# Kernel tuning notes

Hardware: AMD Instinct MI355X
Metric: run time of the kernel (lower is better)

Reference implementation:

```python
import jax, jax.numpy as jnp
import numpy as np

D_MODEL = 64
LN_EPS = 1e-5


def _conv1d(x, w, b, stride, pad):
    # x: (B, Cin, L), w: (Cout, Cin, K)
    y = jax.lax.conv_general_dilated(x, w, (stride,), [(pad, pad)],
                                     dimension_numbers=('NCH', 'OIH', 'NCH'))
    return y + b[None, :, None]


def _layernorm(x, g, b):
    # normalize over last dim (feature dim), matching nn.LayerNorm(d_model)
    m = jnp.mean(x, axis=-1, keepdims=True)
    v = jnp.var(x, axis=-1, keepdims=True)
    return (x - m) * jax.lax.rsqrt(v + LN_EPS) * g + b


def _pos_embed(L, d):
    pos = jnp.arange(L, dtype=jnp.float32)[:, None]
    div = jnp.exp(jnp.arange(0, d, 2, dtype=jnp.float32) * (-np.log(10000.0) / d))
    pe = jnp.zeros((L, d), jnp.float32)
    pe = pe.at[:, 0::2].set(jnp.sin(pos * div))
    pe = pe.at[:, 1::2].set(jnp.cos(pos * div))
    return pe


def setup_inputs():
    key = jax.random.key(0)
    ks = jax.random.split(key, 20)
    B, L, D = 128, 4096, D_MODEL
    G = D // 4  # 16 convs per kernel-size group (kernels cycle [3,5,7,9])
    inp = {'x': jax.random.normal(ks[0], (B, 1, L), jnp.float32)}
    kernels = [3, 5, 7, 9]
    for i, k in enumerate(kernels):
        fan = float(1.0 / np.sqrt(k))
        inp['tok_w%d' % k] = jax.random.uniform(ks[1 + 2 * i], (G, 1, k), jnp.float32, -fan, fan)
        inp['tok_b%d' % k] = jax.random.uniform(ks[2 + 2 * i], (G,), jnp.float32, -fan, fan)
    fan = float(1.0 / np.sqrt(D * 4))
    for j in range(3):
        inp['c_w%d' % (j + 1)] = jax.random.uniform(ks[10 + 2 * j], (D, D, 4), jnp.float32, -fan, fan)
        inp['c_b%d' % (j + 1)] = jax.random.uniform(ks[11 + 2 * j], (D,), jnp.float32, -fan, fan)
    for j in range(2):
        inp['ln_g%d' % (j + 1)] = jnp.ones((D,), jnp.float32)
        inp['ln_b%d' % (j + 1)] = jnp.zeros((D,), jnp.float32)
    return inp


def reference(x, tok_w3, tok_b3, tok_w5, tok_b5, tok_w7, tok_b7, tok_w9, tok_b9,
              c_w1, c_b1, c_w2, c_b2, c_w3, c_b3, ln_g1, ln_b1, ln_g2, ln_b2):
    B, _, L = x.shape
    D = D_MODEL
    # TokenEmbedding: conv i has kernel [3,5,7,9][i%4]; fuse the d_model 1-channel
    # convs into 4 grouped convs (one per kernel size), then interleave channels.
    outs = [
        _conv1d(x, tok_w3, tok_b3, 1, 1),
        _conv1d(x, tok_w5, tok_b5, 1, 2),
        _conv1d(x, tok_w7, tok_b7, 1, 3),
        _conv1d(x, tok_w9, tok_b9, 1, 4),
    ]  # each (B, D//4, L); group g holds channels i with i % 4 == g, ordered by i // 4
    emb = jnp.stack(outs, axis=2).reshape(B, D, L)  # channel i = (i//4)*4 + (i%4)
    # add sinusoidal positional embedding (dropout is identity in eval mode)
    h = emb + _pos_embed(L, D).T[None]  # (B, D, L)
    # CompressionEmbedding: conv(k=4, s=2, p=1) -> tanh -> LN (over D) chain
    h = jnp.tanh(_conv1d(h, c_w1, c_b1, 2, 1))
    h = _layernorm(h.transpose(0, 2, 1), ln_g1, ln_b1).transpose(0, 2, 1)
    h = jnp.tanh(_conv1d(h, c_w2, c_b2, 2, 1))
    h = _layernorm(h.transpose(0, 2, 1), ln_g2, ln_b2).transpose(0, 2, 1)
    h = jnp.tanh(_conv1d(h, c_w3, c_b3, 2, 1))
    return h.transpose(0, 2, 1)  # (B, L//8, D)
```

## Files before the change

kernel.cpp:

```cpp
#include <hip/hip_runtime.h>
#include <math.h>

#define BATCH 128
#define LN_EPS 1e-5f

typedef short bf16x8 __attribute__((ext_vector_type(8)));
typedef short bf16x4 __attribute__((ext_vector_type(4)));
typedef float f32x4  __attribute__((ext_vector_type(4)));

__device__ __forceinline__ ushort f2bf(float f) {
    return __builtin_bit_cast(ushort, (__bf16)f);
}

__device__ __forceinline__ float fast_tanh(float v) {
    float e = __expf(2.f * v);
    return 1.f - 2.f / (e + 1.f);
}

__global__ __launch_bounds__(256, 2)
void prep_kernel(const float* __restrict__ cw1, const float* __restrict__ cw2,
                 const float* __restrict__ cw3,
                 const float* __restrict__ w3, const float* __restrict__ b3,
                 const float* __restrict__ w5, const float* __restrict__ b5,
                 const float* __restrict__ w7, const float* __restrict__ b7,
                 const float* __restrict__ w9, const float* __restrict__ b9,
                 const float* __restrict__ cb1, const float* __restrict__ cb2,
                 const float* __restrict__ cb3,
                 const float* __restrict__ lg1, const float* __restrict__ lb1,
                 const float* __restrict__ lg2, const float* __restrict__ lb2,
                 ushort* __restrict__ Wm23, ushort* __restrict__ Wm1,
                 float* __restrict__ W0c, float* __restrict__ W3c,
                 float* __restrict__ pe1c,
                 float* __restrict__ cb2t, float* __restrict__ B2k0,
                 float* __restrict__ B2k3,
                 float* __restrict__ cb3t, float* __restrict__ B3k0,
                 float* __restrict__ B3k3) {
    const int tid = threadIdx.x;
    const int bx  = blockIdx.x;
    const int idx = bx * 256 + tid;

    __shared__ float tile[64][132];
    __shared__ float red[4][64][24];
    __shared__ float cbred[64][4];

    {
        int s = idx >> 14, r = idx & 16383;
        int j = r & 7, l15 = (r >> 3) & 15, dt = (r >> 7) & 3;
        int quad = (r >> 9) & 3, k2 = (r >> 11) & 1, kk = (r >> 12) & 3;
        int dout = dt * 16 + l15, din = k2 * 32 + quad * 8 + j;
        const float* cw = (s == 0) ? cw2 : cw3;
        const float* lg = (s == 0) ? lg1 : lg2;
        Wm23[idx] = f2bf(cw[dout * 256 + din * 4 + kk] * lg[din]);
    }

    if (bx == 1 && tid < 128) {
        const int s = tid >> 6, ch = tid & 63;
        const float* cw = (s == 0) ? cw2 : cw3;
        const float* lb = (s == 0) ? lb1 : lb2;
        float full = 0.f, k0 = 0.f, k3 = 0.f;
        for (int din = 0; din < 64; ++din) {
            float bv = lb[din];
            const float* wr = cw + ch * 256 + din * 4;
            k0 = fmaf(wr[0], bv, k0);
            k3 = fmaf(wr[3], bv, k3);
            full = fmaf(wr[0] + wr[1] + wr[2] + wr[3], bv, full);
        }
        if (s == 0) { cb2t[ch] = cb2[ch] + full; B2k0[ch] = k0; B2k3[ch] = k3; }
        else        { cb3t[ch] = cb3[ch] + full; B3k0[ch] = k0; B3k3[ch] = k3; }
    }

    if (bx == 0) {
        const int ch = tid & 63, part = tid >> 6;
        const float* cw1row = cw1 + ch * 256;
        float acc[24];
#pragma unroll
        for (int j = 0; j < 24; ++j) acc[j] = 0.f;
        for (int din = part * 16; din < part * 16 + 16; ++din) {
            int ki = din & 3, g = din >> 2;
            float wl[9];
#pragma unroll
            for (int j = 0; j < 9; ++j) wl[j] = 0.f;
            float bias;
            if (ki == 0)      { for (int j = 0; j < 3; ++j) wl[3 + j] = w3[g * 3 + j]; bias = b3[g]; }
            else if (ki == 1) { for (int j = 0; j < 5; ++j) wl[2 + j] = w5[g * 5 + j]; bias = b5[g]; }
            else if (ki == 2) { for (int j = 0; j < 7; ++j) wl[1 + j] = w7[g * 7 + j]; bias = b7[g]; }
            else              { for (int j = 0; j < 9; ++j) wl[j]     = w9[g * 9 + j]; bias = b9[g]; }
#pragma unroll
            for (int kk = 0; kk < 4; ++kk) {
                float c = cw1row[din * 4 + kk];
                acc[12 + kk] += c * bias;
#pragma unroll
                for (int u = 0; u < 9; ++u) acc[kk + u] += c * wl[u];
            }
            float c0 = cw1row[din * 4 + 0], c3 = cw1row[din * 4 + 3];
#pragma unroll
            for (int u = 0; u < 4; ++u) { acc[16 + u] += c0 * wl[5 + u]; acc[20 + u] += c3 * wl[u]; }
        }
#pragma unroll
        for (int j = 0; j < 24; ++j) red[part][ch][j] = acc[j];
    }

    {
        const int pair = tid & 63, part = tid >> 6;
        const int kk = pair >> 4, chl = pair & 15;
        const int ch = (bx & 3) * 16 + chl;
        float s = 0.f;
        for (int din = part * 16; din < part * 16 + 16; ++din) {
            int ki = din & 3, g = din >> 2;
            float bias = (ki == 0) ? b3[g] : (ki == 1) ? b5[g] : (ki == 2) ? b7[g] : b9[g];
            s += cw1[ch * 256 + din * 4 + kk] * bias;
        }
        cbred[pair][part] = s;
    }

    const int l0 = (bx >> 2) * 64;
    const int pin0 = 2 * l0 - 1;
    for (int i2 = tid; i2 < 64 * 130; i2 += 256) {
        int d = i2 / 130, pp = i2 - d * 130;
        int p = pin0 + pp;
        float v = 0.f;
        if (p >= 0 && p < 4096) {
            float dv = __expf((float)(d & ~1) * -0.14391156831212787f);
            float ang = (float)p * dv;
            v = (d & 1) ? __cosf(ang) : __sinf(ang);
        }
        tile[d][pp] = v;
    }
    __syncthreads();

    if (bx == 0 && tid < 64) {
        const int ch = tid;
        float w24[24];
#pragma unroll
        for (int j = 0; j < 24; ++j)
            w24[j] = red[0][ch][j] + red[1][ch][j] + red[2][ch][j] + red[3][ch][j];
        int dt = ch >> 4, l15 = ch & 15;
#pragma unroll
        for (int quad = 0; quad < 4; ++quad)
#pragma unroll
            for (int j = 0; j < 8; ++j) {
                int k = quad * 8 + j;
                Wm1[((quad * 4 + dt) * 16 + l15) * 8 + j] = f2bf(k < 12 ? w24[k] : 0.f);
            }
#pragma unroll
        for (int u = 0; u < 4; ++u) { W0c[ch * 4 + u] = w24[16 + u]; W3c[ch * 4 + u] = w24[20 + u]; }
    }

    const int lane = tid & 63, wv = tid >> 6;
    const int l = l0 + lane;
    const int chl0 = wv * 4;
    const int db = (bx & 3) * 16 + chl0;
    float a4[4];
#pragma unroll
    for (int j = 0; j < 4; ++j) {
        int chl = chl0 + j;
        float cbk0 = cbred[0 * 16 + chl][0] + cbred[0 * 16 + chl][1] + cbred[0 * 16 + chl][2] + cbred[0 * 16 + chl][3];
        float cbk1 = cbred[1 * 16 + chl][0] + cbred[1 * 16 + chl][1] + cbred[1 * 16 + chl][2] + cbred[1 * 16 + chl][3];
        float cbk2 = cbred[2 * 16 + chl][0] + cbred[2 * 16 + chl][1] + cbred[2 * 16 + chl][2] + cbred[2 * 16 + chl][3];
        float cbk3 = cbred[3 * 16 + chl][0] + cbred[3 * 16 + chl][1] + cbred[3 * 16 + chl][2] + cbred[3 * 16 + chl][3];
        float a = cb1[db + j] + cbk1 + cbk2;
        if (l > 0) a += cbk0;
        if (l < 2047) a += cbk3;
        a4[j] = a;
    }
    for (int din = 0; din < 64; ++din) {
        float v0 = tile[din][2 * lane + 0], v1 = tile[din][2 * lane + 1];
        float v2 = tile[din][2 * lane + 2], v3 = tile[din][2 * lane + 3];
        const float* wb = cw1 + din * 4;
#pragma unroll
        for (int j = 0; j < 4; ++j) {
            const float* wj = wb + (db + j) * 256;
            a4[j] = fmaf(v0, wj[0], fmaf(v1, wj[1], fmaf(v2, wj[2], fmaf(v3, wj[3], a4[j]))));
        }
    }
    *(float4*)(pe1c + (size_t)l * 64 + db) = make_float4(a4[0], a4[1], a4[2], a4[3]);
}

__global__ __launch_bounds__(256, 2)
void mega_kernel(const float* __restrict__ x,
                 const ushort* __restrict__ Wm1, const ushort* __restrict__ Wm23,
                 const float* __restrict__ pe1c,
                 const float* __restrict__ W0c, const float* __restrict__ W3c,
                 const float* __restrict__ cb2t, const float* __restrict__ B2k0,
                 const float* __restrict__ B2k3,
                 const float* __restrict__ cb3t, const float* __restrict__ B3k0,
                 const float* __restrict__ B3k3,
                 float* __restrict__ out) {
    const int b = blockIdx.y;
    const int g0 = blockIdx.x * 64;
    const int tid = threadIdx.x;

    __shared__ __align__(16) ushort xs[640];
    __shared__ __align__(16) ushort TE1[148][72];
    __shared__ __align__(16) ushort TO1[148][72];
    __shared__ __align__(16) ushort TE2[66][72];
    __shared__ __align__(16) ushort TO2[66][72];

    for (int i = tid; i < 640; i += 256) {
        int g = 8 * g0 - 11 + i;
        float v = (g >= 0 && g < 4096) ? x[b * 4096 + g] : 0.f;
        xs[i] = f2bf(v);
    }
    __syncthreads();

    const int wv = tid >> 6, lane = tid & 63;
    const int quad = lane >> 4, l15 = lane & 15;

    {
        bf16x8 afr1[4];
#pragma unroll
        for (int dt = 0; dt < 4; ++dt)
            afr1[dt] = *(const bf16x8*)&Wm1[((quad * 4 + dt) * 16 + l15) * 8];
        const int qstart = 4 * g0 - 3;
        for (int pass = wv; pass < 9; pass += 4) {
            const int mb = pass * 32;
            f32x4 a1[2][4];
#pragma unroll
            for (int pt = 0; pt < 2; ++pt) {
                const int m = mb + pt * 16 + l15;
                const int q = qstart + m;
                const int qc = (q < 0) ? 0 : ((q > 2047) ? 2047 : q);
                const float* pb_ = pe1c + (size_t)qc * 64 + quad * 4;
#pragma unroll
                for (int dt = 0; dt < 4; ++dt) {
                    float4 pv = *(const float4*)(pb_ + dt * 16);
                    a1[pt][dt][0] = pv.x; a1[pt][dt][1] = pv.y;
                    a1[pt][dt][2] = pv.z; a1[pt][dt][3] = pv.w;
                }
                union { bf16x8 v; unsigned u[4]; } tmp;
                const unsigned* p = (const unsigned*)&xs[2 * m + 8 * quad];
#pragma unroll
                for (int i = 0; i < 4; ++i) tmp.u[i] = p[i];
#pragma unroll
                for (int dt = 0; dt < 4; ++dt)
                    a1[pt][dt] = __builtin_amdgcn_mfma_f32_16x16x32_bf16(
                        afr1[dt], tmp.v, a1[pt][dt], 0, 0, 0);
            }
#pragma unroll
            for (int pt = 0; pt < 2; ++pt) {
                const int m = mb + pt * 16 + l15;
                if (m >= 264) continue;
                const int q = qstart + m;
                ushort* dst = (m & 1) ? &TE1[(m + 1) >> 1][0] : &TO1[m >> 1][0];
                if (q >= 0 && q < 2048) {
                    if (q == 0 || q == 2047) {
                        const float* Wc = (q == 0) ? W0c : W3c;
                        const float* xe = x + b * 4096 + ((q == 0) ? 0 : 4092);
                        float x0 = xe[0], x1 = xe[1], x2 = xe[2], x3 = xe[3];
#pragma unroll
                        for (int dt = 0; dt < 4; ++dt)
#pragma unroll
                            for (int r = 0; r < 4; ++r) {
                                const float* wc = Wc + (dt * 16 + quad * 4 + r) * 4;
                                a1[pt][dt][r] -= wc[0] * x0 + wc[1] * x1 + wc[2] * x2 + wc[3] * x3;
                            }
                    }
                    float s = 0.f, s2 = 0.f;
#pragma unroll
                    for (int dt = 0; dt < 4; ++dt)
#pragma unroll
                        for (int r = 0; r < 4; ++r) {
                            float t = fast_tanh(a1[pt][dt][r]);
                            s += t;
                            s2 = fmaf(t, t, s2);
                        }
                    s += __shfl_xor(s, 16, 64);
                    s += __shfl_xor(s, 32, 64);
                    s2 += __shfl_xor(s2, 16, 64);
                    s2 += __shfl_xor(s2, 32, 64);
                    float mean = s * 0.015625f;
                    float var = fmaf(-mean, mean, s2 * 0.015625f);
                    float rstd = rsqrtf(var + LN_EPS);
                    float nmr = -mean * rstd;
#pragma unroll
                    for (int dt = 0; dt < 4; ++dt) {
                        bf16x4 pk;
#pragma unroll
                        for (int r = 0; r < 4; ++r)
                            pk[r] = (short)f2bf(fmaf(fast_tanh(a1[pt][dt][r]), rstd, nmr));
                        *(bf16x4*)(dst + dt * 16 + quad * 4) = pk;
                    }
                } else {
                    bf16x4 z; z[0] = 0; z[1] = 0; z[2] = 0; z[3] = 0;
#pragma unroll
                    for (int dt = 0; dt < 4; ++dt)
                        *(bf16x4*)(dst + dt * 16 + quad * 4) = z;
                }
            }
        }
    }
    __syncthreads();

    for (int pass = wv; pass < 9; pass += 4) {
        const int n = pass * 16 + l15;
        f32x4 a2[4];
#pragma unroll
        for (int dt = 0; dt < 4; ++dt) {
            float4 cv = *(const float4*)(cb2t + dt * 16 + quad * 4);
            a2[dt][0] = cv.x; a2[dt][1] = cv.y; a2[dt][2] = cv.z; a2[dt][3] = cv.w;
        }
#pragma unroll
        for (int kk = 0; kk < 4; ++kk) {
            const ushort (*T)[72] = (kk & 1) ? TE1 : TO1;
            const int row = n + ((kk + 1) >> 1);
#pragma unroll
            for (int k2 = 0; k2 < 2; ++k2) {
                bf16x8 bfr = *(const bf16x8*)&T[row][k2 * 32 + quad * 8];
                const ushort* wb = Wm23 + ((((kk * 2 + k2) * 4 + quad) * 4) * 16) * 8;
#pragma unroll
                for (int dt = 0; dt < 4; ++dt) {
                    bf16x8 afr = *(const bf16x8*)(wb + ((size_t)(dt * 16 + l15)) * 8);
                    a2[dt] = __builtin_amdgcn_mfma_f32_16x16x32_bf16(afr, bfr, a2[dt], 0, 0, 0);
                }
            }
        }
        if (n < 130) {
            const int p = 2 * g0 - 1 + n;
            ushort* dst = (n & 1) ? &TE2[(n + 1) >> 1][0] : &TO2[n >> 1][0];
            if (p >= 0 && p < 1024) {
                if (p == 0 || p == 1023) {
                    const float* Bc = (p == 0) ? B2k0 : B2k3;
#pragma unroll
                    for (int dt = 0; dt < 4; ++dt)
#pragma unroll
                        for (int r = 0; r < 4; ++r)
                            a2[dt][r] -= Bc[dt * 16 + quad * 4 + r];
                }
                float s = 0.f, s2 = 0.f;
#pragma unroll
                for (int dt = 0; dt < 4; ++dt)
#pragma unroll
                    for (int r = 0; r < 4; ++r) {
                        float t = fast_tanh(a2[dt][r]);
                        s += t;
                        s2 = fmaf(t, t, s2);
                    }
                s += __shfl_xor(s, 16, 64);
                s += __shfl_xor(s, 32, 64);
                s2 += __shfl_xor(s2, 16, 64);
                s2 += __shfl_xor(s2, 32, 64);
                float mean = s * 0.015625f;
                float var = fmaf(-mean, mean, s2 * 0.015625f);
                float rstd = rsqrtf(var + LN_EPS);
                float nmr = -mean * rstd;
#pragma unroll
                for (int dt = 0; dt < 4; ++dt) {
                    bf16x4 pk;
#pragma unroll
                    for (int r = 0; r < 4; ++r)
                        pk[r] = (short)f2bf(fmaf(fast_tanh(a2[dt][r]), rstd, nmr));
                    *(bf16x4*)(dst + dt * 16 + quad * 4) = pk;
                }
            } else {
                bf16x4 z; z[0] = 0; z[1] = 0; z[2] = 0; z[3] = 0;
#pragma unroll
                for (int dt = 0; dt < 4; ++dt)
                    *(bf16x4*)(dst + dt * 16 + quad * 4) = z;
            }
        }
    }
    __syncthreads();

    {
        const int m3 = wv * 16 + l15;
        f32x4 a3[4];
#pragma unroll
        for (int dt = 0; dt < 4; ++dt) {
            float4 cv = *(const float4*)(cb3t + dt * 16 + quad * 4);
            a3[dt][0] = cv.x; a3[dt][1] = cv.y; a3[dt][2] = cv.z; a3[dt][3] = cv.w;
        }
        const ushort* Wg3 = Wm23 + 16384;
#pragma unroll
        for (int kk = 0; kk < 4; ++kk) {
            const ushort (*T)[72] = (kk & 1) ? TE2 : TO2;
            const int row = m3 + ((kk + 1) >> 1);
#pragma unroll
            for (int k2 = 0; k2 < 2; ++k2) {
                bf16x8 bfr = *(const bf16x8*)&T[row][k2 * 32 + quad * 8];
                const ushort* wb = Wg3 + ((((kk * 2 + k2) * 4 + quad) * 4) * 16) * 8;
#pragma unroll
                for (int dt = 0; dt < 4; ++dt) {
                    bf16x8 afr = *(const bf16x8*)(wb + ((size_t)(dt * 16 + l15)) * 8);
                    a3[dt] = __builtin_amdgcn_mfma_f32_16x16x32_bf16(afr, bfr, a3[dt], 0, 0, 0);
                }
            }
        }
        const int l = g0 + m3;
        if (l == 0 || l == 511) {
            const float* Bc = (l == 0) ? B3k0 : B3k3;
#pragma unroll
            for (int dt = 0; dt < 4; ++dt)
#pragma unroll
                for (int r = 0; r < 4; ++r)
                    a3[dt][r] -= Bc[dt * 16 + quad * 4 + r];
        }
        float* ob = out + ((size_t)(b * 512) + l) * 64;
#pragma unroll
        for (int dt = 0; dt < 4; ++dt) {
            float4 st = make_float4(fast_tanh(a3[dt][0]),
                                    fast_tanh(a3[dt][1]),
                                    fast_tanh(a3[dt][2]),
                                    fast_tanh(a3[dt][3]));
            *(float4*)(ob + dt * 16 + quad * 4) = st;
        }
    }
}

extern "C" void kernel_launch(void* const* d_in, const int* in_sizes, int n_in,
                              void* d_out, int out_size, void* d_ws, size_t ws_size,
                              hipStream_t stream) {
    (void)in_sizes; (void)n_in; (void)out_size; (void)ws_size;
    const float* x   = (const float*)d_in[0];
    const float* w3  = (const float*)d_in[1];
    const float* b3  = (const float*)d_in[2];
    const float* w5  = (const float*)d_in[3];
    const float* b5  = (const float*)d_in[4];
    const float* w7  = (const float*)d_in[5];
    const float* b7  = (const float*)d_in[6];
    const float* w9  = (const float*)d_in[7];
    const float* b9  = (const float*)d_in[8];
    const float* cw1 = (const float*)d_in[9];
    const float* cb1 = (const float*)d_in[10];
    const float* cw2 = (const float*)d_in[11];
    const float* cb2 = (const float*)d_in[12];
    const float* cw3 = (const float*)d_in[13];
    const float* cb3 = (const float*)d_in[14];
    const float* lg1 = (const float*)d_in[15];
    const float* lb1 = (const float*)d_in[16];
    const float* lg2 = (const float*)d_in[17];
    const float* lb2 = (const float*)d_in[18];
    float* out = (float*)d_out;

    char* w = (char*)d_ws;
    ushort* Wm23 = (ushort*)(w + 0);
    ushort* Wm1  = (ushort*)(w + 65536);
    float*  W0c  = (float*)(w + 69632);
    float*  W3c  = (float*)(w + 70656);
    float*  cb2t = (float*)(w + 71680);
    float*  B2k0 = (float*)(w + 71936);
    float*  B2k3 = (float*)(w + 72192);
    float*  cb3t = (float*)(w + 72448);
    float*  B3k0 = (float*)(w + 72704);
    float*  B3k3 = (float*)(w + 72960);
    float*  pe1c = (float*)(w + 73216);

    prep_kernel<<<128, 256, 0, stream>>>(cw1, cw2, cw3, w3, b3, w5, b5, w7, b7, w9, b9,
                                         cb1, cb2, cb3, lg1, lb1, lg2, lb2,
                                         Wm23, Wm1, W0c, W3c, pe1c,
                                         cb2t, B2k0, B2k3, cb3t, B3k0, B3k3);
    mega_kernel<<<dim3(8, BATCH), 256, 0, stream>>>(
        x, Wm1, Wm23, pe1c, W0c, W3c, cb2t, B2k0, B2k3, cb3t, B3k0, B3k3, out);
}
```

Measured before the change: 159.3 us.

## Shrink mega_kernel tiles to one wavefront and 8 outputs per block

Result: slower. 168.5 us (+5.8%).

```diff
diff --git a/kernel.cpp b/kernel.cpp
--- a/kernel.cpp
+++ b/kernel.cpp
@@ -176,7 +176,7 @@
     *(float4*)(pe1c + (size_t)l * 64 + db) = make_float4(a4[0], a4[1], a4[2], a4[3]);
 }
 
-__global__ __launch_bounds__(256, 2)
+__global__ __launch_bounds__(64, 2)
 void mega_kernel(const float* __restrict__ x,
                  const ushort* __restrict__ Wm1, const ushort* __restrict__ Wm23,
                  const float* __restrict__ pe1c,
@@ -187,23 +187,22 @@
                  const float* __restrict__ B3k3,
                  float* __restrict__ out) {
     const int b = blockIdx.y;
-    const int g0 = blockIdx.x * 64;
-    const int tid = threadIdx.x;
-
-    __shared__ __align__(16) ushort xs[640];
-    __shared__ __align__(16) ushort TE1[148][72];
-    __shared__ __align__(16) ushort TO1[148][72];
-    __shared__ __align__(16) ushort TE2[66][72];
-    __shared__ __align__(16) ushort TO2[66][72];
-
-    for (int i = tid; i < 640; i += 256) {
+    const int g0 = blockIdx.x * 8;
+    const int lane = threadIdx.x;
+
+    __shared__ __align__(16) ushort xs[128];
+    __shared__ __align__(16) ushort TE1[21][72];
+    __shared__ __align__(16) ushort TO1[20][72];
+    __shared__ __align__(16) ushort TE2[10][72];
+    __shared__ __align__(16) ushort TO2[9][72];
+
+    for (int i = lane; i < 128; i += 64) {
         int g = 8 * g0 - 11 + i;
         float v = (g >= 0 && g < 4096) ? x[b * 4096 + g] : 0.f;
         xs[i] = f2bf(v);
     }
     __syncthreads();
 
-    const int wv = tid >> 6, lane = tid & 63;
     const int quad = lane >> 4, l15 = lane & 15;
 
     {
@@ -212,35 +211,27 @@
         for (int dt = 0; dt < 4; ++dt)
             afr1[dt] = *(const bf16x8*)&Wm1[((quad * 4 + dt) * 16 + l15) * 8];
         const int qstart = 4 * g0 - 3;
-        for (int pass = wv; pass < 9; pass += 4) {
-            const int mb = pass * 32;
-            f32x4 a1[2][4];
-#pragma unroll
-            for (int pt = 0; pt < 2; ++pt) {
-                const int m = mb + pt * 16 + l15;
-                const int q = qstart + m;
-                const int qc = (q < 0) ? 0 : ((q > 2047) ? 2047 : q);
-                const float* pb_ = pe1c + (size_t)qc * 64 + quad * 4;
-#pragma unroll
-                for (int dt = 0; dt < 4; ++dt) {
-                    float4 pv = *(const float4*)(pb_ + dt * 16);
-                    a1[pt][dt][0] = pv.x; a1[pt][dt][1] = pv.y;
-                    a1[pt][dt][2] = pv.z; a1[pt][dt][3] = pv.w;
-                }
-                union { bf16x8 v; unsigned u[4]; } tmp;
-                const unsigned* p = (const unsigned*)&xs[2 * m + 8 * quad];
-#pragma unroll
-                for (int i = 0; i < 4; ++i) tmp.u[i] = p[i];
-#pragma unroll
-                for (int dt = 0; dt < 4; ++dt)
-                    a1[pt][dt] = __builtin_amdgcn_mfma_f32_16x16x32_bf16(
-                        afr1[dt], tmp.v, a1[pt][dt], 0, 0, 0);
-            }
-#pragma unroll
-            for (int pt = 0; pt < 2; ++pt) {
-                const int m = mb + pt * 16 + l15;
-                if (m >= 264) continue;
-                const int q = qstart + m;
+#pragma unroll
+        for (int pass = 0; pass < 3; ++pass) {
+            const int m = pass * 16 + l15;
+            const int q = qstart + m;
+            const int qc = (q < 0) ? 0 : ((q > 2047) ? 2047 : q);
+            f32x4 a1[4];
+            const float* pb_ = pe1c + (size_t)qc * 64 + quad * 4;
+#pragma unroll
+            for (int dt = 0; dt < 4; ++dt) {
+                float4 pv = *(const float4*)(pb_ + dt * 16);
+                a1[dt][0] = pv.x; a1[dt][1] = pv.y; a1[dt][2] = pv.z; a1[dt][3] = pv.w;
+            }
+            union { bf16x8 v; unsigned u[4]; } tmp;
+            const unsigned* p = (const unsigned*)&xs[2 * m + 8 * quad];
+#pragma unroll
+            for (int i = 0; i < 4; ++i) tmp.u[i] = p[i];
+#pragma unroll
+            for (int dt = 0; dt < 4; ++dt)
+                a1[dt] = __builtin_amdgcn_mfma_f32_16x16x32_bf16(
+                    afr1[dt], tmp.v, a1[dt], 0, 0, 0);
+            if (m < 40) {
                 ushort* dst = (m & 1) ? &TE1[(m + 1) >> 1][0] : &TO1[m >> 1][0];
                 if (q >= 0 && q < 2048) {
                     if (q == 0 || q == 2047) {
@@ -252,7 +243,7 @@
 #pragma unroll
                             for (int r = 0; r < 4; ++r) {
                                 const float* wc = Wc + (dt * 16 + quad * 4 + r) * 4;
-                                a1[pt][dt][r] -= wc[0] * x0 + wc[1] * x1 + wc[2] * x2 + wc[3] * x3;
+                                a1[dt][r] -= wc[0] * x0 + wc[1] * x1 + wc[2] * x2 + wc[3] * x3;
                             }
                     }
                     float s = 0.f, s2 = 0.f;
@@ -260,7 +251,7 @@
                     for (int dt = 0; dt < 4; ++dt)
 #pragma unroll
                         for (int r = 0; r < 4; ++r) {
-                            float t = fast_tanh(a1[pt][dt][r]);
+                            float t = fast_tanh(a1[dt][r]);
                             s += t;
                             s2 = fmaf(t, t, s2);
                         }
@@ -277,7 +268,7 @@
                         bf16x4 pk;
 #pragma unroll
                         for (int r = 0; r < 4; ++r)
-                            pk[r] = (short)f2bf(fmaf(fast_tanh(a1[pt][dt][r]), rstd, nmr));
+                            pk[r] = (short)f2bf(fmaf(fast_tanh(a1[dt][r]), rstd, nmr));
                         *(bf16x4*)(dst + dt * 16 + quad * 4) = pk;
                     }
                 } else {
@@ -291,8 +282,10 @@
     }
     __syncthreads();
 
-    for (int pass = wv; pass < 9; pass += 4) {
+#pragma unroll
+    for (int pass = 0; pass < 2; ++pass) {
         const int n = pass * 16 + l15;
+        const int nc = (n < 18) ? n : 17;
         f32x4 a2[4];
 #pragma unroll
         for (int dt = 0; dt < 4; ++dt) {
@@ -301,11 +294,11 @@
         }
 #pragma unroll
         for (int kk = 0; kk < 4; ++kk) {
-            const ushort (*T)[72] = (kk & 1) ? TE1 : TO1;
-            const int row = n + ((kk + 1) >> 1);
+            const int row = nc + ((kk + 1) >> 1);
+            const ushort* Trow = (kk & 1) ? &TE1[row][0] : &TO1[row][0];
 #pragma unroll
             for (int k2 = 0; k2 < 2; ++k2) {
-                bf16x8 bfr = *(const bf16x8*)&T[row][k2 * 32 + quad * 8];
+                bf16x8 bfr = *(const bf16x8*)(Trow + k2 * 32 + quad * 8);
                 const ushort* wb = Wm23 + ((((kk * 2 + k2) * 4 + quad) * 4) * 16) * 8;
 #pragma unroll
                 for (int dt = 0; dt < 4; ++dt) {
@@ -314,7 +307,7 @@
                 }
             }
         }
-        if (n < 130) {
+        if (n < 18) {
             const int p = 2 * g0 - 1 + n;
             ushort* dst = (n & 1) ? &TE2[(n + 1) >> 1][0] : &TO2[n >> 1][0];
             if (p >= 0 && p < 1024) {
@@ -362,7 +355,8 @@
     __syncthreads();
 
     {
-        const int m3 = wv * 16 + l15;
+        const int m3 = l15;
+        const int m3c = (m3 < 8) ? m3 : 7;
         f32x4 a3[4];
 #pragma unroll
         for (int dt = 0; dt < 4; ++dt) {
@@ -372,11 +366,11 @@
         const ushort* Wg3 = Wm23 + 16384;
 #pragma unroll
         for (int kk = 0; kk < 4; ++kk) {
-            const ushort (*T)[72] = (kk & 1) ? TE2 : TO2;
-            const int row = m3 + ((kk + 1) >> 1);
+            const int row = m3c + ((kk + 1) >> 1);
+            const ushort* Trow = (kk & 1) ? &TE2[row][0] : &TO2[row][0];
 #pragma unroll
             for (int k2 = 0; k2 < 2; ++k2) {
-                bf16x8 bfr = *(const bf16x8*)&T[row][k2 * 32 + quad * 8];
+                bf16x8 bfr = *(const bf16x8*)(Trow + k2 * 32 + quad * 8);
                 const ushort* wb = Wg3 + ((((kk * 2 + k2) * 4 + quad) * 4) * 16) * 8;
 #pragma unroll
                 for (int dt = 0; dt < 4; ++dt) {
@@ -385,23 +379,25 @@
                 }
             }
         }
-        const int l = g0 + m3;
-        if (l == 0 || l == 511) {
-            const float* Bc = (l == 0) ? B3k0 : B3k3;
-#pragma unroll
-            for (int dt = 0; dt < 4; ++dt)
-#pragma unroll
-                for (int r = 0; r < 4; ++r)
-                    a3[dt][r] -= Bc[dt * 16 + quad * 4 + r];
-        }
-        float* ob = out + ((size_t)(b * 512) + l) * 64;
-#pragma unroll
-        for (int dt = 0; dt < 4; ++dt) {
-            float4 st = make_float4(fast_tanh(a3[dt][0]),
-                                    fast_tanh(a3[dt][1]),
-                                    fast_tanh(a3[dt][2]),
-                                    fast_tanh(a3[dt][3]));
-            *(float4*)(ob + dt * 16 + quad * 4) = st;
+        if (m3 < 8) {
+            const int l = g0 + m3;
+            if (l == 0 || l == 511) {
+                const float* Bc = (l == 0) ? B3k0 : B3k3;
+#pragma unroll
+                for (int dt = 0; dt < 4; ++dt)
+#pragma unroll
+                    for (int r = 0; r < 4; ++r)
+                        a3[dt][r] -= Bc[dt * 16 + quad * 4 + r];
+            }
+            float* ob = out + ((size_t)(b * 512) + l) * 64;
+#pragma unroll
+            for (int dt = 0; dt < 4; ++dt) {
+                float4 st = make_float4(fast_tanh(a3[dt][0]),
+                                        fast_tanh(a3[dt][1]),
+                                        fast_tanh(a3[dt][2]),
+                                        fast_tanh(a3[dt][3]));
+                *(float4*)(ob + dt * 16 + quad * 4) = st;
+            }
         }
     }
 }
@@ -448,6 +444,6 @@
                                          cb1, cb2, cb3, lg1, lb1, lg2, lb2,
                                          Wm23, Wm1, W0c, W3c, pe1c,
                                          cb2t, B2k0, B2k3, cb3t, B3k0, B3k3);
-    mega_kernel<<<dim3(8, BATCH), 256, 0, stream>>>(
+    mega_kernel<<<dim3(64, BATCH), 64, 0, stream>>>(
         x, Wm1, Wm23, pe1c, W0c, W3c, cb2t, B2k0, B2k3, cb3t, B3k0, B3k3, out);
 }
```
